# Kernel tuning notes

Measured on AMD Instinct MI355X. Metric: run time of the kernel, lower is better.

Reference implementation:

```python
import jax, jax.numpy as jnp
import numpy as np

B, H, SQ, SK, D = 2, 16, 2048, 2048, 128
P_DROP = 0.5


def setup_inputs() -> dict:
    key = jax.random.key(0)
    kq, kk, kv, km = jax.random.split(key, 4)
    query = jax.random.normal(kq, (B, H, SQ, D), dtype=jnp.float32)
    key_t = jax.random.normal(kk, (B, H, SK, D), dtype=jnp.float32)
    value = jax.random.normal(kv, (B, H, SK, D), dtype=jnp.float32)
    # deterministic Bernoulli(0.5) keep-mask standing in for dropout(p=0.5, train=True)
    dropout_mask = jax.random.randint(km, (B, H, SQ, SK), 0, 2, dtype=jnp.int32)
    return {"query": query, "key": key_t, "value": value, "dropout_mask": dropout_mask}


def reference(query, key, value, dropout_mask):
    d = query.shape[-1]
    # original: scaled_qk = qk.div(d ** -0.5)  ==  qk * sqrt(d)  (faithful to source)
    scale = jnp.asarray(d, query.dtype) ** 0.5
    qk = jnp.einsum("bhqd,bhkd->bhqk", query, key)  # [B,H,SQ,SK]
    scaled_qk = qk * scale
    keep_scale = jnp.asarray(1.0 / (1.0 - P_DROP), query.dtype)
    dropped = jnp.where(dropout_mask == 1, scaled_qk * keep_scale, jnp.zeros((), query.dtype))
    out = jnp.einsum("bhqk,bhkd->bhqd", dropped, value)  # [B,H,SQ,D]
    return out
```

## Files before the change

kernel.cpp:

```cpp
#include <hip/hip_runtime.h>
#include <hip/hip_bf16.h>

#define B_   2
#define H_   16
#define SQ_  2048
#define SK_  2048
#define D_   128

#define QT   128
#define KT   64
#define NITER (SK_/KT)

using bf16x8 = __attribute__((ext_vector_type(8))) __bf16;
using bf16x4 = __attribute__((ext_vector_type(4))) __bf16;
using f32x4  = __attribute__((ext_vector_type(4))) float;

#define MFMA16(a,b,c) __builtin_amdgcn_mfma_f32_16x16x32_bf16(a,b,c,0,0,0)

#define QK_PITCH 136
#define VT_PITCH 72
#define P_PITCH  72
#define M8_PITCH 72

#define KLDS_BYTES (KT  * QK_PITCH * 2)
#define VT_BYTES   (D_  * VT_PITCH * 2)
#define P_BYTES    (QT  * P_PITCH  * 2)
#define M8_BYTES   (QT  * M8_PITCH)
#define SMEM_BYTES (KLDS_BYTES + VT_BYTES + P_BYTES + M8_BYTES)

__global__ __launch_bounds__(256, 2)
void attn_drop_kernel(const float* __restrict__ Q,
                      const float* __restrict__ K,
                      const float* __restrict__ V,
                      const int*   __restrict__ M,
                      float* __restrict__ Out)
{
    __shared__ __align__(16) char smem[SMEM_BYTES];
    __bf16*  Qs  = (__bf16*)smem;
    __bf16*  Ks  = (__bf16*)smem;
    __bf16*  Vt  = (__bf16*)(smem + KLDS_BYTES);
    __bf16*  Ps  = (__bf16*)(smem + KLDS_BYTES + VT_BYTES);
    unsigned char* Ms8 = (unsigned char*)(smem + KLDS_BYTES + VT_BYTES + P_BYTES);

    const int tid  = threadIdx.x;
    const int wave = tid >> 6;
    const int lane = tid & 63;
    const int quad = lane >> 4;
    const int ln   = lane & 15;

    const int orig = ((blockIdx.x & 7) << 6) | (blockIdx.x >> 3);
    const int bh = orig >> 4;
    const int qb = orig & 15;

    const float* qptr = Q + ((size_t)bh*SQ_ + (size_t)qb*QT) * D_;
    const float* kptr = K + (size_t)bh*SK_*D_;
    const float* vptr = V + (size_t)bh*SK_*D_;
    const int*   mptr = M + (size_t)bh*(size_t)SQ_*SK_ + (size_t)qb*QT*SK_;
    float*       optr = Out + ((size_t)bh*SQ_ + (size_t)qb*QT) * D_;

    const int c  = tid & 31;
    const int g  = tid >> 5;
    const int mc = tid & 15;
    const int mg = tid >> 4;

    float4 kpre[8], vpre[8];
    int4   mpre[8];

    auto load_tile = [&](int kt) {
        const float4* ks = (const float4*)(kptr + (size_t)kt*KT*D_);
        const float4* vs = (const float4*)(vptr + (size_t)kt*KT*D_);
        #pragma unroll
        for (int p = 0; p < 8; ++p) kpre[p] = ks[(g + 8*p)*32 + c];
        #pragma unroll
        for (int i = 0; i < 8; ++i) vpre[i] = vs[(8*g + i)*32 + c];
        const int* mrow = mptr + kt*KT + 4*mc;
        #pragma unroll
        for (int p = 0; p < 8; ++p)
            mpre[p] = *(const int4*)(mrow + (size_t)(mg + 16*p)*SK_);
    };

    auto write_tile = [&]() {
        #pragma unroll
        for (int p = 0; p < 8; ++p) {
            float4 v = kpre[p];
            bf16x4 h = { (__bf16)v.x, (__bf16)v.y, (__bf16)v.z, (__bf16)v.w };
            *(bf16x4*)&Ks[(g + 8*p)*QK_PITCH + 4*c] = h;
        }
        const float* ff = (const float*)vpre;
        #pragma unroll
        for (int j = 0; j < 4; ++j) {
            bf16x8 row = { (__bf16)ff[0*4+j], (__bf16)ff[1*4+j],
                           (__bf16)ff[2*4+j], (__bf16)ff[3*4+j],
                           (__bf16)ff[4*4+j], (__bf16)ff[5*4+j],
                           (__bf16)ff[6*4+j], (__bf16)ff[7*4+j] };
            *(bf16x8*)&Vt[(4*c + j)*VT_PITCH + 8*g] = row;
        }
        #pragma unroll
        for (int p = 0; p < 8; ++p) {
            int4 m = mpre[p];
            unsigned pk = (unsigned)(m.x & 1) | ((unsigned)(m.y & 1) << 8)
                        | ((unsigned)(m.z & 1) << 16) | ((unsigned)(m.w & 1) << 24);
            *(unsigned*)&Ms8[(mg + 16*p)*M8_PITCH + 4*mc] = pk;
        }
    };

    load_tile(0);

    {
        const float4* src = (const float4*)qptr;
        #pragma unroll
        for (int p = 0; p < 16; ++p) {
            int r = g + 8*p;
            float4 v = src[r*32 + c];
            bf16x4 h = { (__bf16)v.x, (__bf16)v.y, (__bf16)v.z, (__bf16)v.w };
            *(bf16x4*)&Qs[r*QK_PITCH + 4*c] = h;
        }
    }
    __syncthreads();

    bf16x8 qf[2][4];
    #pragma unroll
    for (int rt = 0; rt < 2; ++rt)
        #pragma unroll
        for (int s = 0; s < 4; ++s)
            qf[rt][s] = *(const bf16x8*)&Qs[(32*wave + 16*rt + ln)*QK_PITCH + 32*s + 8*quad];

    f32x4 Oacc[2][8];
    #pragma unroll
    for (int rt = 0; rt < 2; ++rt)
        #pragma unroll
        for (int dt = 0; dt < 8; ++dt)
            Oacc[rt][dt] = (f32x4){0.f, 0.f, 0.f, 0.f};

    for (int kt = 0; kt < NITER; ++kt) {
        __syncthreads();
        write_tile();
        __syncthreads();
        if (kt + 1 < NITER) load_tile(kt + 1);

        f32x4 S[2][4];
        #pragma unroll
        for (int rt = 0; rt < 2; ++rt)
            #pragma unroll
            for (int ct = 0; ct < 4; ++ct)
                S[rt][ct] = (f32x4){0.f, 0.f, 0.f, 0.f};

        __builtin_amdgcn_s_setprio(1);
        #pragma unroll
        for (int s = 0; s < 4; ++s) {
            #pragma unroll
            for (int ct = 0; ct < 4; ++ct) {
                bf16x8 kf = *(const bf16x8*)&Ks[(16*ct + ln)*QK_PITCH + 32*s + 8*quad];
                S[0][ct] = MFMA16(qf[0][s], kf, S[0][ct]);
                S[1][ct] = MFMA16(qf[1][s], kf, S[1][ct]);
            }
        }
        __builtin_amdgcn_s_setprio(0);

        #pragma unroll
        for (int rt = 0; rt < 2; ++rt) {
            #pragma unroll
            for (int ct = 0; ct < 4; ++ct) {
                int row0 = 32*wave + 16*rt + 4*quad;
                int col  = 16*ct + ln;
                #pragma unroll
                for (int r = 0; r < 4; ++r) {
                    float pv = Ms8[(row0 + r)*M8_PITCH + col] ? S[rt][ct][r] : 0.0f;
                    Ps[(row0 + r)*P_PITCH + col] = (__bf16)pv;
                }
            }
        }

        __builtin_amdgcn_s_setprio(1);
        #pragma unroll
        for (int ks = 0; ks < 2; ++ks) {
            bf16x8 pf0 = *(const bf16x8*)&Ps[(32*wave +      ln)*P_PITCH + 32*ks + 8*quad];
            bf16x8 pf1 = *(const bf16x8*)&Ps[(32*wave + 16 + ln)*P_PITCH + 32*ks + 8*quad];
            #pragma unroll
            for (int dt = 0; dt < 8; ++dt) {
                bf16x8 vf = *(const bf16x8*)&Vt[(16*dt + ln)*VT_PITCH + 32*ks + 8*quad];
                Oacc[0][dt] = MFMA16(pf0, vf, Oacc[0][dt]);
                Oacc[1][dt] = MFMA16(pf1, vf, Oacc[1][dt]);
            }
        }
        __builtin_amdgcn_s_setprio(0);
    }

    const float SCALE = 22.62741699796952f;
    #pragma unroll
    for (int rt = 0; rt < 2; ++rt) {
        #pragma unroll
        for (int dt = 0; dt < 8; ++dt) {
            int row0 = 32*wave + 16*rt + 4*quad;
            #pragma unroll
            for (int r = 0; r < 4; ++r)
                optr[(size_t)(row0 + r)*D_ + 16*dt + ln] = Oacc[rt][dt][r] * SCALE;
        }
    }
}

extern "C" void kernel_launch(void* const* d_in, const int* in_sizes, int n_in,
                              void* d_out, int out_size, void* d_ws, size_t ws_size,
                              hipStream_t stream) {
    (void)in_sizes; (void)n_in; (void)d_ws; (void)ws_size; (void)out_size;
    const float* Q = (const float*)d_in[0];
    const float* K = (const float*)d_in[1];
    const float* V = (const float*)d_in[2];
    const int*   M = (const int*)d_in[3];
    float* Out = (float*)d_out;

    dim3 grid(B_ * H_ * (SQ_ / QT));
    attn_drop_kernel<<<grid, 256, 0, stream>>>(Q, K, V, M, Out);
}
```

Before: 890.9 us.

## Use 8 waves per block with 16 query rows each

Doubles the block from 256 to 512 threads, so each wave owns 16 query rows instead of 32. Tile loads are split across twice as many threads, which halves the per-thread prefetch registers and the accumulator state. The aim is more waves in flight to hide global-load and LDS latency. In exchange, each K and V fragment read from LDS now feeds half as many MFMAs, and barriers must coordinate more waves.

```diff
diff --git a/kernel.cpp b/kernel.cpp
--- a/kernel.cpp
+++ b/kernel.cpp
@@ -28,7 +28,7 @@
 #define M8_BYTES   (QT  * M8_PITCH)
 #define SMEM_BYTES (KLDS_BYTES + VT_BYTES + P_BYTES + M8_BYTES)
 
-__global__ __launch_bounds__(256, 2)
+__global__ __launch_bounds__(512, 4)
 void attn_drop_kernel(const float* __restrict__ Q,
                       const float* __restrict__ K,
                       const float* __restrict__ V,
@@ -63,44 +63,42 @@
     const int mc = tid & 15;
     const int mg = tid >> 4;
 
-    float4 kpre[8], vpre[8];
-    int4   mpre[8];
+    float4 kpre[4], vpre[4];
+    int4   mpre[4];
 
     auto load_tile = [&](int kt) {
         const float4* ks = (const float4*)(kptr + (size_t)kt*KT*D_);
         const float4* vs = (const float4*)(vptr + (size_t)kt*KT*D_);
         #pragma unroll
-        for (int p = 0; p < 8; ++p) kpre[p] = ks[(g + 8*p)*32 + c];
+        for (int p = 0; p < 4; ++p) kpre[p] = ks[(g + 16*p)*32 + c];
         #pragma unroll
-        for (int i = 0; i < 8; ++i) vpre[i] = vs[(8*g + i)*32 + c];
+        for (int i = 0; i < 4; ++i) vpre[i] = vs[(4*g + i)*32 + c];
         const int* mrow = mptr + kt*KT + 4*mc;
         #pragma unroll
-        for (int p = 0; p < 8; ++p)
-            mpre[p] = *(const int4*)(mrow + (size_t)(mg + 16*p)*SK_);
+        for (int p = 0; p < 4; ++p)
+            mpre[p] = *(const int4*)(mrow + (size_t)(mg + 32*p)*SK_);
     };
 
     auto write_tile = [&]() {
         #pragma unroll
-        for (int p = 0; p < 8; ++p) {
+        for (int p = 0; p < 4; ++p) {
             float4 v = kpre[p];
             bf16x4 h = { (__bf16)v.x, (__bf16)v.y, (__bf16)v.z, (__bf16)v.w };
-            *(bf16x4*)&Ks[(g + 8*p)*QK_PITCH + 4*c] = h;
+            *(bf16x4*)&Ks[(g + 16*p)*QK_PITCH + 4*c] = h;
         }
         const float* ff = (const float*)vpre;
         #pragma unroll
         for (int j = 0; j < 4; ++j) {
-            bf16x8 row = { (__bf16)ff[0*4+j], (__bf16)ff[1*4+j],
-                           (__bf16)ff[2*4+j], (__bf16)ff[3*4+j],
-                           (__bf16)ff[4*4+j], (__bf16)ff[5*4+j],
-                           (__bf16)ff[6*4+j], (__bf16)ff[7*4+j] };
-            *(bf16x8*)&Vt[(4*c + j)*VT_PITCH + 8*g] = row;
+            bf16x4 row = { (__bf16)ff[0*4+j], (__bf16)ff[1*4+j],
+                           (__bf16)ff[2*4+j], (__bf16)ff[3*4+j] };
+            *(bf16x4*)&Vt[(4*c + j)*VT_PITCH + 4*g] = row;
         }
         #pragma unroll
-        for (int p = 0; p < 8; ++p) {
+        for (int p = 0; p < 4; ++p) {
             int4 m = mpre[p];
             unsigned pk = (unsigned)(m.x & 1) | ((unsigned)(m.y & 1) << 8)
                         | ((unsigned)(m.z & 1) << 16) | ((unsigned)(m.w & 1) << 24);
-            *(unsigned*)&Ms8[(mg + 16*p)*M8_PITCH + 4*mc] = pk;
+            *(unsigned*)&Ms8[(mg + 32*p)*M8_PITCH + 4*mc] = pk;
         }
     };
 
@@ -109,8 +107,8 @@
     {
         const float4* src = (const float4*)qptr;
         #pragma unroll
-        for (int p = 0; p < 16; ++p) {
-            int r = g + 8*p;
+        for (int p = 0; p < 8; ++p) {
+            int r = g + 16*p;
             float4 v = src[r*32 + c];
             bf16x4 h = { (__bf16)v.x, (__bf16)v.y, (__bf16)v.z, (__bf16)v.w };
             *(bf16x4*)&Qs[r*QK_PITCH + 4*c] = h;
@@ -118,19 +116,15 @@
     }
     __syncthreads();
 
-    bf16x8 qf[2][4];
+    bf16x8 qf[4];
     #pragma unroll
-    for (int rt = 0; rt < 2; ++rt)
-        #pragma unroll
-        for (int s = 0; s < 4; ++s)
-            qf[rt][s] = *(const bf16x8*)&Qs[(32*wave + 16*rt + ln)*QK_PITCH + 32*s + 8*quad];
+    for (int s = 0; s < 4; ++s)
+        qf[s] = *(const bf16x8*)&Qs[(16*wave + ln)*QK_PITCH + 32*s + 8*quad];
 
-    f32x4 Oacc[2][8];
+    f32x4 Oacc[8];
     #pragma unroll
-    for (int rt = 0; rt < 2; ++rt)
-        #pragma unroll
-        for (int dt = 0; dt < 8; ++dt)
-            Oacc[rt][dt] = (f32x4){0.f, 0.f, 0.f, 0.f};
+    for (int dt = 0; dt < 8; ++dt)
+        Oacc[dt] = (f32x4){0.f, 0.f, 0.f, 0.f};
 
     for (int kt = 0; kt < NITER; ++kt) {
         __syncthreads();
@@ -138,12 +132,10 @@
         __syncthreads();
         if (kt + 1 < NITER) load_tile(kt + 1);
 
-        f32x4 S[2][4];
+        f32x4 S[4];
         #pragma unroll
-        for (int rt = 0; rt < 2; ++rt)
-            #pragma unroll
-            for (int ct = 0; ct < 4; ++ct)
-                S[rt][ct] = (f32x4){0.f, 0.f, 0.f, 0.f};
+        for (int ct = 0; ct < 4; ++ct)
+            S[ct] = (f32x4){0.f, 0.f, 0.f, 0.f};
 
         __builtin_amdgcn_s_setprio(1);
         #pragma unroll
@@ -151,36 +143,30 @@
             #pragma unroll
             for (int ct = 0; ct < 4; ++ct) {
                 bf16x8 kf = *(const bf16x8*)&Ks[(16*ct + ln)*QK_PITCH + 32*s + 8*quad];
-                S[0][ct] = MFMA16(qf[0][s], kf, S[0][ct]);
-                S[1][ct] = MFMA16(qf[1][s], kf, S[1][ct]);
+                S[ct] = MFMA16(qf[s], kf, S[ct]);
             }
         }
         __builtin_amdgcn_s_setprio(0);
 
         #pragma unroll
-        for (int rt = 0; rt < 2; ++rt) {
+        for (int ct = 0; ct < 4; ++ct) {
+            int row0 = 16*wave + 4*quad;
+            int col  = 16*ct + ln;
             #pragma unroll
-            for (int ct = 0; ct < 4; ++ct) {
-                int row0 = 32*wave + 16*rt + 4*quad;
-                int col  = 16*ct + ln;
-                #pragma unroll
-                for (int r = 0; r < 4; ++r) {
-                    float pv = Ms8[(row0 + r)*M8_PITCH + col] ? S[rt][ct][r] : 0.0f;
-                    Ps[(row0 + r)*P_PITCH + col] = (__bf16)pv;
-                }
+            for (int r = 0; r < 4; ++r) {
+                float pv = Ms8[(row0 + r)*M8_PITCH + col] ? S[ct][r] : 0.0f;
+                Ps[(row0 + r)*P_PITCH + col] = (__bf16)pv;
             }
         }
 
         __builtin_amdgcn_s_setprio(1);
         #pragma unroll
         for (int ks = 0; ks < 2; ++ks) {
-            bf16x8 pf0 = *(const bf16x8*)&Ps[(32*wave +      ln)*P_PITCH + 32*ks + 8*quad];
-            bf16x8 pf1 = *(const bf16x8*)&Ps[(32*wave + 16 + ln)*P_PITCH + 32*ks + 8*quad];
+            bf16x8 pf = *(const bf16x8*)&Ps[(16*wave + ln)*P_PITCH + 32*ks + 8*quad];
             #pragma unroll
             for (int dt = 0; dt < 8; ++dt) {
                 bf16x8 vf = *(const bf16x8*)&Vt[(16*dt + ln)*VT_PITCH + 32*ks + 8*quad];
-                Oacc[0][dt] = MFMA16(pf0, vf, Oacc[0][dt]);
-                Oacc[1][dt] = MFMA16(pf1, vf, Oacc[1][dt]);
+                Oacc[dt] = MFMA16(pf, vf, Oacc[dt]);
             }
         }
         __builtin_amdgcn_s_setprio(0);
@@ -188,14 +174,11 @@
 
     const float SCALE = 22.62741699796952f;
     #pragma unroll
-    for (int rt = 0; rt < 2; ++rt) {
+    for (int dt = 0; dt < 8; ++dt) {
+        int row0 = 16*wave + 4*quad;
         #pragma unroll
-        for (int dt = 0; dt < 8; ++dt) {
-            int row0 = 32*wave + 16*rt + 4*quad;
-            #pragma unroll
-            for (int r = 0; r < 4; ++r)
-                optr[(size_t)(row0 + r)*D_ + 16*dt + ln] = Oacc[rt][dt][r] * SCALE;
-        }
+        for (int r = 0; r < 4; ++r)
+            optr[(size_t)(row0 + r)*D_ + 16*dt + ln] = Oacc[dt][r] * SCALE;
     }
 }
 
@@ -210,5 +193,5 @@
     float* Out = (float*)d_out;
 
     dim3 grid(B_ * H_ * (SQ_ / QT));
-    attn_drop_kernel<<<grid, 256, 0, stream>>>(Q, K, V, M, Out);
+    attn_drop_kernel<<<grid, 512, 0, stream>>>(Q, K, V, M, Out);
 }
```

Result: slower. 948.0 us (+6.4%).
